# Performance work log

Measured on AMD Instinct MI355X. Metric: run time of the kernel, lower is better.

## Reference

```python
import jax, jax.numpy as jnp
import numpy as np

EPS = 1e-5  # BatchNorm eps (eval mode, running_mean=0, running_var=1)


def conv1x1(x, w):
    # x: [n,c,h,w], w: [o,c]
    return jnp.einsum('nchw,oc->nohw', x, w)


def bn_relu(x, s, b):
    scale = s / jnp.sqrt(1.0 + EPS)
    return jax.nn.relu(x * scale[None, :, None, None] + b[None, :, None, None])


def upsample_bilinear_ac(x, out_h, out_w):
    # nn.Upsample(mode='bilinear', align_corners=True)
    n, c, h, w = x.shape
    ys = jnp.linspace(0.0, h - 1.0, out_h)
    xs = jnp.linspace(0.0, w - 1.0, out_w)
    y0 = jnp.floor(ys).astype(jnp.int32)
    y1 = jnp.minimum(y0 + 1, h - 1)
    x0 = jnp.floor(xs).astype(jnp.int32)
    x1 = jnp.minimum(x0 + 1, w - 1)
    wy = (ys - y0)[None, None, :, None]
    wx = (xs - x0)[None, None, None, :]
    rows = x[:, :, y0, :] * (1.0 - wy) + x[:, :, y1, :] * wy
    return rows[:, :, :, x0] * (1.0 - wx) + rows[:, :, :, x1] * wx


def to_patches(x, ph, pw):
    # [n,c,H,W] -> [n,c,P,L], P = (H//ph)*(W//pw) patches, L = ph*pw pixels
    n, c, H, W = x.shape
    gh, gw = H // ph, W // pw
    return x.reshape(n, c, gh, ph, gw, pw).transpose(0, 1, 2, 4, 3, 5).reshape(n, c, gh * gw, ph * pw)


def from_patches(x, H, W, ph, pw):
    n, c, P, L = x.shape
    gh, gw = H // ph, W // pw
    return x.reshape(n, c, gh, gw, ph, pw).transpose(0, 1, 2, 4, 3, 5).reshape(n, c, H, W)


def patch_attention(q, k, v, ph, pw, H, W):
    qp = to_patches(q, ph, pw)
    kp = to_patches(k, ph, pw)
    vp = to_patches(v, ph, pw)
    # patch-vs-patch similarity, contracted over pixels within a patch
    sim = jax.nn.sigmoid(jnp.einsum('ncpl,ncql->ncpq', qp, kp))
    # sim1 (mean over key patches) + sim2 (mean over query patches), both [n,c,P,1]
    gate = sim.mean(axis=3, keepdims=True) + sim.mean(axis=2)[..., None]
    return from_patches(gate * vp, H, W, ph, pw)


def setup_inputs() -> dict:
    key = jax.random.key(0)
    ks = jax.random.split(key, 20)
    N, Ch, Cl, neck = 8, 256, 512, 64
    H = W = 128
    Hs = Ws = 32
    sc = 0.05
    return {
        'branch0_feats': jax.random.normal(ks[0], (N, Ch, H, W), jnp.float32),
        'other_feats': jax.random.normal(ks[1], (N, Cl, Hs, Ws), jnp.float32),
        'wq1': jax.random.normal(ks[2], (neck, Ch), jnp.float32) * sc,
        'bnq1_s': jax.random.uniform(ks[3], (neck,), jnp.float32, 0.5, 1.5),
        'bnq1_b': jax.random.normal(ks[4], (neck,), jnp.float32) * 0.1,
        'wk1': jax.random.normal(ks[5], (neck, Cl), jnp.float32) * sc,
        'bnk1_s': jax.random.uniform(ks[6], (neck,), jnp.float32, 0.5, 1.5),
        'bnk1_b': jax.random.normal(ks[7], (neck,), jnp.float32) * 0.1,
        'wv1': jax.random.normal(ks[8], (neck, Ch), jnp.float32) * sc,
        'wq2': jax.random.normal(ks[9], (neck, Ch), jnp.float32) * sc,
        'bnq2_s': jax.random.uniform(ks[10], (neck,), jnp.float32, 0.5, 1.5),
        'bnq2_b': jax.random.normal(ks[11], (neck,), jnp.float32) * 0.1,
        'wk2': jax.random.normal(ks[12], (neck, Cl), jnp.float32) * sc,
        'bnk2_s': jax.random.uniform(ks[13], (neck,), jnp.float32, 0.5, 1.5),
        'bnk2_b': jax.random.normal(ks[14], (neck,), jnp.float32) * 0.1,
        'wz': jax.random.normal(ks[15], (Ch, 2 * neck), jnp.float32) * sc,
        'alpha': jax.random.uniform(ks[16], (1,), jnp.float32),
        'gamma': jax.random.uniform(ks[17], (1,), jnp.float32),
    }


def reference(branch0_feats, other_feats, wq1, bnq1_s, bnq1_b, wk1, bnk1_s, bnk1_b, wv1,
              wq2, bnq2_s, bnq2_b, wk2, bnk2_s, bnk2_b, wz, alpha, gamma):
    _, _, H, W = branch0_feats.shape
    _, _, Hs, Ws = other_feats.shape

    value = conv1x1(branch0_feats, wv1)
    query = bn_relu(conv1x1(branch0_feats, wq1), bnq1_s, bnq1_b)
    key = upsample_bilinear_ac(bn_relu(conv1x1(other_feats, wk1), bnk1_s, bnk1_b), H, W)

    half = query.shape[1] // 2
    # scale 1: patches of size (Hs, Ws)
    ctx0 = patch_attention(query[:, :half], key[:, :half], value[:, :half], Hs, Ws, H, W)
    # scale 2: patches of size (Hs//2, Ws//2)
    ctx2 = patch_attention(query[:, half:], key[:, half:], value[:, half:], Hs // 2, Ws // 2, H, W)

    # dense per-pixel sigmoid gating branch
    query2 = bn_relu(conv1x1(branch0_feats, wq2), bnq2_s, bnq2_b)
    key2 = upsample_bilinear_ac(bn_relu(conv1x1(other_feats, wk2), bnk2_s, bnk2_b), H, W)
    ctx3 = value * jax.nn.sigmoid(query2 * key2)

    context = jnp.concatenate([alpha[0] * jnp.concatenate([ctx0, ctx2], axis=1),
                               gamma[0] * ctx3], axis=1)
    return conv1x1(context, wz)
```

## Files before the change

### kernel.cpp

```cpp
#include <hip/hip_runtime.h>
#include <math.h>
#include <stdint.h>

#define N_    8
#define CH    256
#define CL    512
#define NECK  64
#define H_    128
#define W_    128
#define HW    16384
#define HWS   1024
#define EPSB  1e-5f
#define SC31  (31.0f/127.0f)

typedef unsigned short ushort_t;
typedef __attribute__((ext_vector_type(8))) short bf16x8;
typedef __attribute__((ext_vector_type(4))) float f32x4;

union bfpack { ushort_t u[8]; bf16x8 v; };

__device__ __forceinline__ float sigmoidf_(float x){ return 1.0f/(1.0f + __expf(-x)); }

__device__ __forceinline__ ushort_t f2bf(float x){
    union { float f; uint32_t u; } v; v.f = x;
    uint32_t r = (v.u + 0x7FFFu + ((v.u >> 16) & 1u)) >> 16;
    return (ushort_t)r;
}
__device__ __forceinline__ float bf2f(ushort_t b){
    union { uint32_t u; float f; } v; v.u = ((uint32_t)b) << 16;
    return v.f;
}

__device__ __forceinline__ void gload16(const void* g, void* l){
    __builtin_amdgcn_global_load_lds((const __attribute__((address_space(1))) void*)g,
                                     (__attribute__((address_space(3))) void*)l, 16, 0, 0);
}

__global__ __launch_bounds__(256) void k_conv_small_prep(
    const float* __restrict__ x,
    const float* __restrict__ wk1, const float* __restrict__ wk2,
    const float* __restrict__ sk1, const float* __restrict__ bk1,
    const float* __restrict__ sk2, const float* __restrict__ bk2,
    const float* __restrict__ wv1, const float* __restrict__ wq1, const float* __restrict__ wq2,
    const float* __restrict__ wz,
    float* __restrict__ k1small, float* __restrict__ k2small,
    ushort_t* __restrict__ Wbig, ushort_t* __restrict__ Wzb)
{
    __shared__ float xt[64][64];
    __shared__ float wt[64][132];
    if (blockIdx.x >= 128){
        int t = (blockIdx.x - 128)*256 + threadIdx.x;
        if (t < 49152){
            int o = t >> 8, c = t & 255;
            const float* w = (o < 64) ? (wv1 + (size_t)o*CH)
                           : (o < 128) ? (wq1 + (size_t)(o-64)*CH)
                                       : (wq2 + (size_t)(o-128)*CH);
            Wbig[t] = f2bf(w[c]);
        } else {
            int i = t - 49152;
            Wzb[i] = f2bf(wz[i]);
        }
        return;
    }
    int T = blockIdx.x;
    int n = T >> 4;
    int pix0 = (T & 15) * 64;
    int t = threadIdx.x;
    int to = t >> 4;
    int tp = t & 15;
    float acc[8][4];
    #pragma unroll
    for (int i=0;i<8;i++){ acc[i][0]=0.f;acc[i][1]=0.f;acc[i][2]=0.f;acc[i][3]=0.f; }

    const float* xb = x + (size_t)n*CL*HWS + pix0;
    for (int cc=0; cc<8; ++cc){
        #pragma unroll
        for (int i=0;i<16;i++){
            int e = i*256 + t;
            int c = e >> 6, p = e & 63;
            xt[c][p] = xb[(size_t)(cc*64 + c)*HWS + p];
        }
        #pragma unroll
        for (int i=0;i<32;i++){
            int e = i*256 + t;
            int o = e >> 6, c = e & 63;
            const float* wsrc = (o < 64) ? (wk1 + (size_t)o*CL) : (wk2 + (size_t)(o-64)*CL);
            wt[c][o] = wsrc[cc*64 + c];
        }
        __syncthreads();
        #pragma unroll 4
        for (int c=0;c<64;c++){
            float4 xv = *(const float4*)&xt[c][tp*4];
            const float4* wr = (const float4*)&wt[c][to*8];
            float4 wa = wr[0], wb = wr[1];
            float wv[8] = {wa.x,wa.y,wa.z,wa.w, wb.x,wb.y,wb.z,wb.w};
            #pragma unroll
            for (int i=0;i<8;i++){
                acc[i][0] = fmaf(wv[i], xv.x, acc[i][0]);
                acc[i][1] = fmaf(wv[i], xv.y, acc[i][1]);
                acc[i][2] = fmaf(wv[i], xv.z, acc[i][2]);
                acc[i][3] = fmaf(wv[i], xv.w, acc[i][3]);
            }
        }
        __syncthreads();
    }
    float inv = rsqrtf(1.0f + EPSB);
    #pragma unroll
    for (int i=0;i<8;i++){
        int o = to*8 + i;
        int g = o >> 6, oc = o & 63;
        float sc = (g ? sk2[oc] : sk1[oc]) * inv;
        float bb =  g ? bk2[oc] : bk1[oc];
        float4 r;
        r.x = fmaxf(fmaf(acc[i][0],sc,bb), 0.f);
        r.y = fmaxf(fmaf(acc[i][1],sc,bb), 0.f);
        r.z = fmaxf(fmaf(acc[i][2],sc,bb), 0.f);
        r.w = fmaxf(fmaf(acc[i][3],sc,bb), 0.f);
        float* dst = g ? k2small : k1small;
        *(float4*)&dst[(size_t)(n*NECK + oc)*HWS + pix0 + tp*4] = r;
    }
}

__global__ __launch_bounds__(512) void k_gemm_big(
    const float* __restrict__ x,
    const ushort_t* __restrict__ Wb,
    const float* __restrict__ s1, const float* __restrict__ b1,
    const float* __restrict__ s2, const float* __restrict__ b2,
    ushort_t* __restrict__ value, ushort_t* __restrict__ query, ushort_t* __restrict__ query2)
{
    __shared__ ushort_t At[192*64];
    __shared__ ushort_t Bt[128*64];
    int blk = blockIdx.x;
    int n = blk >> 7;
    int pix0 = (blk & 127) << 7;
    int t = threadIdx.x;
    int lane = t & 63;
    int w8 = t >> 6;
    int wm = w8 >> 1, wn = w8 & 1;

    f32x4 acc[3][4];
    #pragma unroll
    for (int m=0;m<3;m++)
        #pragma unroll
        for (int nn=0;nn<4;nn++) acc[m][nn] = (f32x4){0.f,0.f,0.f,0.f};

    const float* xb = x + (size_t)n*CH*HW + pix0;
    float va[8], vb[8];
    {
        const float* xc = xb + (size_t)(8*w8)*HW;
        #pragma unroll
        for (int j=0;j<8;j++){
            va[j] = xc[(size_t)j*HW + lane];
            vb[j] = xc[(size_t)j*HW + 64 + lane];
        }
    }
    for (int kt=0; kt<4; ++kt){
        int c0 = kt*64;
        #pragma unroll
        for (int i=0;i<3;i++){
            int g = i*512 + t;
            int s = g ^ ((g>>3)&7);
            gload16(Wb + (size_t)(s>>3)*CH + c0 + (s&7)*8, (char*)At + g*16);
        }
        uint32_t pa[4], pb[4];
        #pragma unroll
        for (int j=0;j<4;j++){
            pa[j] = (uint32_t)f2bf(va[2*j]) | ((uint32_t)f2bf(va[2*j+1]) << 16);
            pb[j] = (uint32_t)f2bf(vb[2*j]) | ((uint32_t)f2bf(vb[2*j+1]) << 16);
        }
        int c2 = (8*w8)*2;
        int offA = (lane*128 + c2) ^ ((lane&7)<<4);
        int offB = ((lane+64)*128 + c2) ^ ((lane&7)<<4);
        *(uint4*)((char*)Bt + offA) = make_uint4(pa[0],pa[1],pa[2],pa[3]);
        *(uint4*)((char*)Bt + offB) = make_uint4(pb[0],pb[1],pb[2],pb[3]);
        __syncthreads();
        if (kt < 3){
            const float* xc = xb + (size_t)((kt+1)*64 + 8*w8)*HW;
            #pragma unroll
            for (int j=0;j<8;j++){
                va[j] = xc[(size_t)j*HW + lane];
                vb[j] = xc[(size_t)j*HW + 64 + lane];
            }
        }
        #pragma unroll
        for (int ks=0; ks<2; ++ks){
            bf16x8 a[3], b[4];
            #pragma unroll
            for (int m=0;m<3;m++){
                int row = wm*48 + m*16 + (lane&15);
                int off = (row*128 + ks*64 + (lane>>4)*16) ^ ((row&7)<<4);
                a[m] = *(const bf16x8*)((const char*)At + off);
            }
            #pragma unroll
            for (int nn=0;nn<4;nn++){
                int row = wn*64 + nn*16 + (lane&15);
                int off = (row*128 + ks*64 + (lane>>4)*16) ^ ((row&7)<<4);
                b[nn] = *(const bf16x8*)((const char*)Bt + off);
            }
            #pragma unroll
            for (int m=0;m<3;m++)
                #pragma unroll
                for (int nn=0;nn<4;nn++)
                    acc[m][nn] = __builtin_amdgcn_mfma_f32_16x16x32_bf16(a[m], b[nn], acc[m][nn], 0, 0, 0);
        }
        __syncthreads();
    }
    float inv = rsqrtf(1.0f + EPSB);
    #pragma unroll
    for (int m=0;m<3;m++){
        int obase = wm*48 + m*16 + ((lane>>4)<<2);
        #pragma unroll
        for (int r=0;r<4;r++){
            int o = obase + r;
            int grp = o >> 6, oc = o & 63;
            float sc = 1.f, bb = 0.f;
            ushort_t* dst;
            if (grp == 0) dst = value;
            else if (grp == 1){ sc = s1[oc]*inv; bb = b1[oc]; dst = query; }
            else              { sc = s2[oc]*inv; bb = b2[oc]; dst = query2; }
            #pragma unroll
            for (int nn=0;nn<4;nn++){
                int pix = pix0 + wn*64 + nn*16 + (lane&15);
                float v = acc[m][nn][r];
                if (grp) v = fmaxf(fmaf(v, sc, bb), 0.f);
                dst[((size_t)(n*NECK + oc))*HW + pix] = f2bf(v);
            }
        }
    }
}

__global__ __launch_bounds__(256) void k_gates(
    const ushort_t* __restrict__ query, const float* __restrict__ k1small,
    float* __restrict__ gate1, float* __restrict__ gate2)
{
    __shared__ __align__(16) char smem[69632];
    int bid = blockIdx.x;
    int t = threadIdx.x;
    int lane = t & 63, wv = t >> 6;
    int r16 = lane & 15, g = lane >> 4;
    float* ksm = (float*)smem;
    ushort_t* qt = (ushort_t*)(smem + 4096);
    ushort_t* kt = (ushort_t*)(smem + 4096 + 32768);

    if (bid < 256){
        int n = bid >> 5, c = bid & 31;
        const float* ks = k1small + (size_t)(n*NECK + c)*HWS;
        #pragma unroll
        for (int i=0;i<4;i++) ksm[i*256+t] = ks[i*256+t];
        __syncthreads();
        const ushort_t* qb = query + (size_t)(n*NECK + c)*HW;
        #pragma unroll
        for (int i=0;i<8;i++){
            int task = i*256 + t;
            int p = task >> 7, c8 = task & 127;
            int ly = c8 >> 2, lx8 = (c8 & 3)*8;
            int h = (p>>2)*32 + ly, w = (p&3)*32 + lx8;
            bf16x8 qv = *(const bf16x8*)(qb + h*W_ + w);
            int off = (p*2048 + c8*16) ^ ((p&7)<<4);
            *(bf16x8*)((char*)qt + off) = qv;
            float yf = h*SC31; int y0=(int)yf; int y1=min(y0+1,31); float fy=yf-(float)y0;
            bfpack pk;
            #pragma unroll
            for (int j=0;j<8;j++){
                int ww = w + j;
                float xf = ww*SC31; int x0=(int)xf; int x1=min(x0+1,31); float fx=xf-(float)x0;
                float a=ksm[y0*32+x0], b=ksm[y0*32+x1], cc=ksm[y1*32+x0], d=ksm[y1*32+x1];
                float r0=a+(b-a)*fx, r1=cc+(d-cc)*fx;
                pk.u[j] = f2bf(r0 + (r1-r0)*fy);
            }
            *(bf16x8*)((char*)kt + off) = pk.v;
        }
        __syncthreads();
        f32x4 acc = (f32x4){0.f,0.f,0.f,0.f};
        #pragma unroll
        for (int k8=0; k8<8; ++k8){
            int l0 = wv*256 + k8*32 + g*8;
            int off = (r16*2048 + l0*2) ^ ((r16&7)<<4);
            bf16x8 av = *(const bf16x8*)((char*)qt + off);
            bf16x8 bv = *(const bf16x8*)((char*)kt + off);
            acc = __builtin_amdgcn_mfma_f32_16x16x32_bf16(av, bv, acc, 0, 0, 0);
        }
        __syncthreads();
        float* pw = (float*)smem;
        #pragma unroll
        for (int r=0;r<4;r++)
            pw[wv*256 + (g*4+r)*16 + r16] = acc[r];
        __syncthreads();
        float* simM = (float*)(smem + 4096);
        float s = pw[t] + pw[256+t] + pw[512+t] + pw[768+t];
        simM[t] = sigmoidf_(s);
        __syncthreads();
        if (t < 16){
            float rs=0.f, cs=0.f;
            #pragma unroll
            for (int q=0;q<16;q++) rs += simM[t*16+q];
            #pragma unroll
            for (int p=0;p<16;p++) cs += simM[p*16+t];
            gate1[(size_t)(n*32 + c)*16 + t] = (rs + cs) * (1.0f/16.0f);
        }
    } else {
        int b2 = bid - 256;
        int n = b2 >> 5, cl = b2 & 31, c = 32 + cl;
        const float* ks = k1small + (size_t)(n*NECK + c)*HWS;
        #pragma unroll
        for (int i=0;i<4;i++) ksm[i*256+t] = ks[i*256+t];
        __syncthreads();
        const ushort_t* qb = query + (size_t)(n*NECK + c)*HW;
        #pragma unroll
        for (int i=0;i<8;i++){
            int task = i*256 + t;
            int p = task >> 5, c8 = task & 31;
            int ly = c8 >> 1, lx8 = (c8 & 1)*8;
            int h = (p>>3)*16 + ly, w = (p&7)*16 + lx8;
            bf16x8 qv = *(const bf16x8*)(qb + h*W_ + w);
            int off = (p*512 + c8*16) ^ ((p&7)<<4);
            *(bf16x8*)((char*)qt + off) = qv;
            float yf = h*SC31; int y0=(int)yf; int y1=min(y0+1,31); float fy=yf-(float)y0;
            bfpack pk;
            #pragma unroll
            for (int j=0;j<8;j++){
                int ww = w + j;
                float xf = ww*SC31; int x0=(int)xf; int x1=min(x0+1,31); float fx=xf-(float)x0;
                float a=ksm[y0*32+x0], b=ksm[y0*32+x1], cc=ksm[y1*32+x0], d=ksm[y1*32+x1];
                float r0=a+(b-a)*fx, r1=cc+(d-cc)*fx;
                pk.u[j] = f2bf(r0 + (r1-r0)*fy);
            }
            *(bf16x8*)((char*)kt + off) = pk.v;
        }
        __syncthreads();
        f32x4 acc2[4];
        #pragma unroll
        for (int qc=0;qc<4;qc++) acc2[qc] = (f32x4){0.f,0.f,0.f,0.f};
        #pragma unroll
        for (int k8=0; k8<8; ++k8){
            int l0 = k8*32 + g*8;
            int offA = ((wv*16 + r16)*512 + l0*2) ^ ((r16&7)<<4);
            bf16x8 av = *(const bf16x8*)((char*)qt + offA);
            #pragma unroll
            for (int qc=0;qc<4;qc++){
                int offB = ((qc*16 + r16)*512 + l0*2) ^ ((r16&7)<<4);
                bf16x8 bv = *(const bf16x8*)((char*)kt + offB);
                acc2[qc] = __builtin_amdgcn_mfma_f32_16x16x32_bf16(av, bv, acc2[qc], 0, 0, 0);
            }
        }
        __syncthreads();
        float* simM = (float*)smem;
        #pragma unroll
        for (int qc=0;qc<4;qc++)
            #pragma unroll
            for (int r=0;r<4;r++){
                int p = wv*16 + g*4 + r, q = qc*16 + r16;
                simM[p*65 + q] = sigmoidf_(acc2[qc][r]);
            }
        __syncthreads();
        if (t < 64){
            float rs=0.f, cs=0.f;
            for (int q=0;q<64;q++) rs += simM[t*65 + q];
            for (int p=0;p<64;p++) cs += simM[p*65 + t];
            gate2[(size_t)(n*32 + cl)*64 + t] = (rs + cs) * (1.0f/64.0f);
        }
    }
}

__global__ __launch_bounds__(512, 4) void k_final_mfma(
    const ushort_t* __restrict__ value, const ushort_t* __restrict__ query2,
    const float* __restrict__ k2small,
    const float* __restrict__ gate1, const float* __restrict__ gate2,
    const ushort_t* __restrict__ Wzb,
    const float* __restrict__ alpha_p, const float* __restrict__ gamma_p,
    float* __restrict__ out)
{
    __shared__ __align__(16) char smem[59392];
    ushort_t* Ct = (ushort_t*)smem;
    float* g1s = (float*)(smem + 32768);
    float* g2s = (float*)(smem + 34816);
    float* k2r = (float*)(smem + 43008);
    int blk = blockIdx.x;
    int n = blk >> 7, h = blk & 127;
    int pix0 = h << 7;
    int t = threadIdx.x;
    int lane = t & 63;
    int wid = t >> 6;
    int wm = wid >> 1, wn = wid & 1;

    int px = t & 127, qd = t >> 7;
    const size_t vbase = (size_t)n*NECK*HW + pix0 + px;
    ushort_t vreg[16], qreg[16];
    #pragma unroll
    for (int i=0;i<16;i++){
        int c = qd*16 + i;
        vreg[i] = value [vbase + (size_t)c*HW];
        qreg[i] = query2[vbase + (size_t)c*HW];
    }

    float alpha = alpha_p[0], gamma = gamma_p[0];
    g1s[t & 511] = gate1[(size_t)n*512 + (t & 511)];
    #pragma unroll
    for (int i=0;i<4;i++) g2s[i*512 + t] = gate2[(size_t)n*2048 + i*512 + t];

    float yf = h * SC31;
    int y0 = (int)yf, y1 = min(y0+1, 31);
    float fy = yf - (float)y0;
    #pragma unroll
    for (int i=0;i<8;i++){
        int e = i*512 + t;
        int buf = e >> 11, c = (e >> 5) & 63, xx = e & 31;
        k2r[buf*2048 + c*32 + xx] = k2small[((size_t)n*NECK + c)*HWS + (buf ? y1 : y0)*32 + xx];
    }
    __syncthreads();

    float xf = px * SC31;
    int x0 = (int)xf, x1 = min(x0+1, 31);
    float fx = xf - (float)x0;
    int patch1 = (h>>5)*4 + (px>>5);
    int patch2 = (h>>4)*8 + (px>>4);
    #pragma unroll
    for (int j=0;j<2;j++){
        bfpack pk;
        #pragma unroll
        for (int i=0;i<8;i++){
            int ch = qd*16 + j*8 + i;
            float g = (ch < 32) ? g1s[ch*16 + patch1] : g2s[(ch-32)*64 + patch2];
            pk.u[i] = f2bf(alpha * g * bf2f(vreg[j*8+i]));
        }
        int off = (px*256 + qd*32 + j*16) ^ ((px&7)<<4);
        *(bf16x8*)((char*)Ct + off) = pk.v;
    }
    #pragma unroll
    for (int j=0;j<2;j++){
        bfpack pk;
        #pragma unroll
        for (int i=0;i<8;i++){
            int c = qd*16 + j*8 + i;
            float vv = bf2f(vreg[j*8+i]);
            float q2 = bf2f(qreg[j*8+i]);
            float r0 = k2r[c*32+x0];      r0 += (k2r[c*32+x1] - r0)*fx;
            float r1 = k2r[2048+c*32+x0]; r1 += (k2r[2048+c*32+x1] - r1)*fx;
            float kv = r0 + (r1 - r0)*fy;
            pk.u[i] = f2bf(gamma * vv * sigmoidf_(q2*kv));
        }
        int off = (px*256 + 128 + qd*32 + j*16) ^ ((px&7)<<4);
        *(bf16x8*)((char*)Ct + off) = pk.v;
    }
    __syncthreads();

    f32x4 acc[4][4];
    #pragma unroll
    for (int m=0;m<4;m++)
        #pragma unroll
        for (int nn=0;nn<4;nn++) acc[m][nn] = (f32x4){0.f,0.f,0.f,0.f};
    #pragma unroll
    for (int ks=0; ks<4; ++ks){
        bf16x8 a[4], b[4];
        #pragma unroll
        for (int m=0;m<4;m++){
            int row = wm*64 + m*16 + (lane&15);
            a[m] = *(const bf16x8*)(Wzb + row*128 + ks*32 + (lane>>4)*8);
        }
        #pragma unroll
        for (int nn=0;nn<4;nn++){
            int row = wn*64 + nn*16 + (lane&15);
            int off = (row*256 + ks*64 + (lane>>4)*16) ^ ((row&7)<<4);
            b[nn] = *(const bf16x8*)((const char*)Ct + off);
        }
        #pragma unroll
        for (int m=0;m<4;m++)
            #pragma unroll
            for (int nn=0;nn<4;nn++)
                acc[m][nn] = __builtin_amdgcn_mfma_f32_16x16x32_bf16(a[m], b[nn], acc[m][nn], 0, 0, 0);
    }

    #pragma unroll
    for (int m=0;m<4;m++){
        int obase = wm*64 + m*16 + ((lane>>4)<<2);
        #pragma unroll
        for (int r=0;r<4;r++){
            int o = obase + r;
            float* dst = out + ((size_t)(n*CH + o))*HW + pix0 + wn*64 + (lane&15);
            #pragma unroll
            for (int nn=0;nn<4;nn++)
                dst[nn*16] = acc[m][nn][r];
        }
    }
}

extern "C" void kernel_launch(void* const* d_in, const int* in_sizes, int n_in,
                              void* d_out, int out_size, void* d_ws, size_t ws_size,
                              hipStream_t stream) {
    const float* x0  = (const float*)d_in[0];
    const float* xo  = (const float*)d_in[1];
    const float* wq1 = (const float*)d_in[2];
    const float* s1  = (const float*)d_in[3];
    const float* b1  = (const float*)d_in[4];
    const float* wk1 = (const float*)d_in[5];
    const float* sk1 = (const float*)d_in[6];
    const float* bk1 = (const float*)d_in[7];
    const float* wv1 = (const float*)d_in[8];
    const float* wq2 = (const float*)d_in[9];
    const float* s2  = (const float*)d_in[10];
    const float* b2  = (const float*)d_in[11];
    const float* wk2 = (const float*)d_in[12];
    const float* sk2 = (const float*)d_in[13];
    const float* bk2 = (const float*)d_in[14];
    const float* wz  = (const float*)d_in[15];
    const float* alp = (const float*)d_in[16];
    const float* gam = (const float*)d_in[17];

    ushort_t* value  = (ushort_t*)d_ws;
    ushort_t* query  = value  + 8388608;
    ushort_t* query2 = query  + 8388608;
    float*    k1s    = (float*)(query2 + 8388608);
    float*    k2s    = k1s + 524288;
    float*    g1     = k2s + 524288;
    float*    g2     = g1 + 4096;
    ushort_t* Wbig   = (ushort_t*)(g2 + 16384);
    ushort_t* Wzb    = Wbig + 49152;

    k_conv_small_prep<<<dim3(448), dim3(256), 0, stream>>>(
        xo, wk1, wk2, sk1, bk1, sk2, bk2, wv1, wq1, wq2, wz, k1s, k2s, Wbig, Wzb);
    k_gemm_big<<<dim3(1024), dim3(512), 0, stream>>>(
        x0, Wbig, s1, b1, s2, b2, value, query, query2);
    k_gates<<<dim3(512), dim3(256), 0, stream>>>(query, k1s, g1, g2);
    k_final_mfma<<<dim3(1024), dim3(512), 0, stream>>>(value, query2, k2s, g1, g2, Wzb,
                                                       alp, gam, (float*)d_out);
}
```

Measured before the change: 153.3 us.

## Merge small conv, big GEMM and weight prep into one phase-1 kernel

Fuses the small key convolutions, the weight bf16 conversion and the large value/query GEMM into a single launch, using block-index ranges to pick the role. The big GEMM now loads fp32 weights directly and converts them in registers instead of reading a prebuilt bf16 weight buffer, which removes the dependency on a prep kernel. The small key convolution moves from fp32 FMA to bf16 MFMA. This saves one launch and a serial dependency, and costs redundant weight conversion in every block plus reduced precision for the key path.

```diff
diff --git a/kernel.cpp b/kernel.cpp
--- a/kernel.cpp
+++ b/kernel.cpp
@@ -1,4 +1,5 @@
 #include <hip/hip_runtime.h>
+#include <hip/hip_bf16.h>
 #include <math.h>
 #include <stdint.h>
 
@@ -22,121 +23,149 @@
 __device__ __forceinline__ float sigmoidf_(float x){ return 1.0f/(1.0f + __expf(-x)); }
 
 __device__ __forceinline__ ushort_t f2bf(float x){
-    union { float f; uint32_t u; } v; v.f = x;
-    uint32_t r = (v.u + 0x7FFFu + ((v.u >> 16) & 1u)) >> 16;
-    return (ushort_t)r;
+    union { __hip_bfloat16 h; ushort_t u; } cv;
+    cv.h = __float2bfloat16(x);
+    return cv.u;
+}
+__device__ __forceinline__ uint32_t pack2(float lo, float hi){
+    return (uint32_t)f2bf(lo) | ((uint32_t)f2bf(hi) << 16);
 }
 __device__ __forceinline__ float bf2f(ushort_t b){
     union { uint32_t u; float f; } v; v.u = ((uint32_t)b) << 16;
     return v.f;
 }
 
-__device__ __forceinline__ void gload16(const void* g, void* l){
-    __builtin_amdgcn_global_load_lds((const __attribute__((address_space(1))) void*)g,
-                                     (__attribute__((address_space(3))) void*)l, 16, 0, 0);
-}
-
-__global__ __launch_bounds__(256) void k_conv_small_prep(
+__global__ __launch_bounds__(512) void k_phase1(
     const float* __restrict__ x,
+    const float* __restrict__ xo,
+    const float* __restrict__ wv1, const float* __restrict__ wq1, const float* __restrict__ wq2,
     const float* __restrict__ wk1, const float* __restrict__ wk2,
+    const float* __restrict__ s1, const float* __restrict__ b1,
+    const float* __restrict__ s2, const float* __restrict__ b2,
     const float* __restrict__ sk1, const float* __restrict__ bk1,
     const float* __restrict__ sk2, const float* __restrict__ bk2,
-    const float* __restrict__ wv1, const float* __restrict__ wq1, const float* __restrict__ wq2,
     const float* __restrict__ wz,
-    float* __restrict__ k1small, float* __restrict__ k2small,
-    ushort_t* __restrict__ Wbig, ushort_t* __restrict__ Wzb)
+    ushort_t* __restrict__ value, ushort_t* __restrict__ query, ushort_t* __restrict__ query2,
+    float* __restrict__ k1s, float* __restrict__ k2s, ushort_t* __restrict__ Wzb)
 {
-    __shared__ float xt[64][64];
-    __shared__ float wt[64][132];
-    if (blockIdx.x >= 128){
-        int t = (blockIdx.x - 128)*256 + threadIdx.x;
-        if (t < 49152){
-            int o = t >> 8, c = t & 255;
-            const float* w = (o < 64) ? (wv1 + (size_t)o*CH)
-                           : (o < 128) ? (wq1 + (size_t)(o-64)*CH)
-                                       : (wq2 + (size_t)(o-128)*CH);
-            Wbig[t] = f2bf(w[c]);
-        } else {
-            int i = t - 49152;
-            Wzb[i] = f2bf(wz[i]);
-        }
+    __shared__ __align__(16) char smem[40960];
+    int blk = blockIdx.x;
+    int t = threadIdx.x;
+
+    if (blk >= 1088){
+        int i = (blk - 1088)*2048 + t*4;
+        float4 f = *(const float4*)(wz + i);
+        *(uint2*)(Wzb + i) = make_uint2(pack2(f.x,f.y), pack2(f.z,f.w));
         return;
     }
-    int T = blockIdx.x;
-    int n = T >> 4;
-    int pix0 = (T & 15) * 64;
-    int t = threadIdx.x;
-    int to = t >> 4;
-    int tp = t & 15;
-    float acc[8][4];
-    #pragma unroll
-    for (int i=0;i<8;i++){ acc[i][0]=0.f;acc[i][1]=0.f;acc[i][2]=0.f;acc[i][3]=0.f; }
-
-    const float* xb = x + (size_t)n*CL*HWS + pix0;
-    for (int cc=0; cc<8; ++cc){
-        #pragma unroll
-        for (int i=0;i<16;i++){
-            int e = i*256 + t;
-            int c = e >> 6, p = e & 63;
-            xt[c][p] = xb[(size_t)(cc*64 + c)*HWS + p];
-        }
-        #pragma unroll
-        for (int i=0;i<32;i++){
-            int e = i*256 + t;
-            int o = e >> 6, c = e & 63;
-            const float* wsrc = (o < 64) ? (wk1 + (size_t)o*CL) : (wk2 + (size_t)(o-64)*CL);
-            wt[c][o] = wsrc[cc*64 + c];
-        }
-        __syncthreads();
-        #pragma unroll 4
-        for (int c=0;c<64;c++){
-            float4 xv = *(const float4*)&xt[c][tp*4];
-            const float4* wr = (const float4*)&wt[c][to*8];
-            float4 wa = wr[0], wb = wr[1];
-            float wv[8] = {wa.x,wa.y,wa.z,wa.w, wb.x,wb.y,wb.z,wb.w};
-            #pragma unroll
-            for (int i=0;i<8;i++){
-                acc[i][0] = fmaf(wv[i], xv.x, acc[i][0]);
-                acc[i][1] = fmaf(wv[i], xv.y, acc[i][1]);
-                acc[i][2] = fmaf(wv[i], xv.z, acc[i][2]);
-                acc[i][3] = fmaf(wv[i], xv.w, acc[i][3]);
-            }
-        }
-        __syncthreads();
-    }
+
+    int lane = t & 63, w8 = t >> 6;
+    int wm = w8 >> 1, wn = w8 & 1;
+    int r16 = lane & 15;
     float inv = rsqrtf(1.0f + EPSB);
-    #pragma unroll
-    for (int i=0;i<8;i++){
-        int o = to*8 + i;
-        int g = o >> 6, oc = o & 63;
-        float sc = (g ? sk2[oc] : sk1[oc]) * inv;
-        float bb =  g ? bk2[oc] : bk1[oc];
-        float4 r;
-        r.x = fmaxf(fmaf(acc[i][0],sc,bb), 0.f);
-        r.y = fmaxf(fmaf(acc[i][1],sc,bb), 0.f);
-        r.z = fmaxf(fmaf(acc[i][2],sc,bb), 0.f);
-        r.w = fmaxf(fmaf(acc[i][3],sc,bb), 0.f);
-        float* dst = g ? k2small : k1small;
-        *(float4*)&dst[(size_t)(n*NECK + oc)*HWS + pix0 + tp*4] = r;
-    }
-}
-
-__global__ __launch_bounds__(512) void k_gemm_big(
-    const float* __restrict__ x,
-    const ushort_t* __restrict__ Wb,
-    const float* __restrict__ s1, const float* __restrict__ b1,
-    const float* __restrict__ s2, const float* __restrict__ b2,
-    ushort_t* __restrict__ value, ushort_t* __restrict__ query, ushort_t* __restrict__ query2)
-{
-    __shared__ ushort_t At[192*64];
-    __shared__ ushort_t Bt[128*64];
-    int blk = blockIdx.x;
+
+    if (blk >= 1024){
+        ushort_t* At = (ushort_t*)smem;
+        ushort_t* Bt = (ushort_t*)(smem + 16384);
+        int b = blk - 1024;
+        int n = b >> 3, pix0 = (b & 7) << 7;
+        f32x4 acc[2][4];
+        #pragma unroll
+        for (int m=0;m<2;m++)
+            #pragma unroll
+            for (int nn=0;nn<4;nn++) acc[m][nn] = (f32x4){0.f,0.f,0.f,0.f};
+
+        const float* xb = xo + (size_t)n*CL*HWS + pix0;
+        float va[8], vb[8];
+        {
+            const float* xc = xb + (size_t)(8*w8)*HWS;
+            #pragma unroll
+            for (int j=0;j<8;j++){
+                va[j] = xc[(size_t)j*HWS + lane];
+                vb[j] = xc[(size_t)j*HWS + 64 + lane];
+            }
+        }
+        int oo = t >> 3, c8 = t & 7;
+        for (int kt=0; kt<8; ++kt){
+            int c0 = kt*64;
+            const float* ws0 = wk1 + (size_t)oo*CL + c0 + c8*8;
+            const float* ws1 = wk2 + (size_t)oo*CL + c0 + c8*8;
+            float4 a00 = *(const float4*)ws0, a01 = *(const float4*)(ws0+4);
+            float4 a10 = *(const float4*)ws1, a11 = *(const float4*)(ws1+4);
+            uint32_t pa[4], pb[4];
+            #pragma unroll
+            for (int j=0;j<4;j++){
+                pa[j] = pack2(va[2*j], va[2*j+1]);
+                pb[j] = pack2(vb[2*j], vb[2*j+1]);
+            }
+            int offA = (lane*128 + w8*16) ^ ((lane&7)<<4);
+            int offB = ((lane+64)*128 + w8*16) ^ ((lane&7)<<4);
+            *(uint4*)((char*)Bt + offA) = make_uint4(pa[0],pa[1],pa[2],pa[3]);
+            *(uint4*)((char*)Bt + offB) = make_uint4(pb[0],pb[1],pb[2],pb[3]);
+            {
+                int off0 = (oo*128 + c8*16) ^ ((oo&7)<<4);
+                int off1 = ((64+oo)*128 + c8*16) ^ ((oo&7)<<4);
+                *(uint4*)((char*)At + off0) = make_uint4(pack2(a00.x,a00.y),pack2(a00.z,a00.w),
+                                                         pack2(a01.x,a01.y),pack2(a01.z,a01.w));
+                *(uint4*)((char*)At + off1) = make_uint4(pack2(a10.x,a10.y),pack2(a10.z,a10.w),
+                                                         pack2(a11.x,a11.y),pack2(a11.z,a11.w));
+            }
+            __syncthreads();
+            if (kt < 7){
+                const float* xc = xb + (size_t)((kt+1)*64 + 8*w8)*HWS;
+                #pragma unroll
+                for (int j=0;j<8;j++){
+                    va[j] = xc[(size_t)j*HWS + lane];
+                    vb[j] = xc[(size_t)j*HWS + 64 + lane];
+                }
+            }
+            #pragma unroll
+            for (int ks=0; ks<2; ++ks){
+                bf16x8 a[2], bfr[4];
+                #pragma unroll
+                for (int m=0;m<2;m++){
+                    int row = wm*32 + m*16 + r16;
+                    int off = (row*128 + ks*64 + (lane>>4)*16) ^ ((row&7)<<4);
+                    a[m] = *(const bf16x8*)((const char*)At + off);
+                }
+                #pragma unroll
+                for (int nn=0;nn<4;nn++){
+                    int row = wn*64 + nn*16 + r16;
+                    int off = (row*128 + ks*64 + (lane>>4)*16) ^ ((row&7)<<4);
+                    bfr[nn] = *(const bf16x8*)((const char*)Bt + off);
+                }
+                #pragma unroll
+                for (int m=0;m<2;m++)
+                    #pragma unroll
+                    for (int nn=0;nn<4;nn++)
+                        acc[m][nn] = __builtin_amdgcn_mfma_f32_16x16x32_bf16(a[m], bfr[nn], acc[m][nn], 0, 0, 0);
+            }
+            __syncthreads();
+        }
+        #pragma unroll
+        for (int m=0;m<2;m++){
+            int obase = wm*32 + m*16 + ((lane>>4)<<2);
+            #pragma unroll
+            for (int r=0;r<4;r++){
+                int o = obase + r;
+                int oc = o & 63;
+                float sc = ((o<64) ? sk1[oc] : sk2[oc]) * inv;
+                float bb =  (o<64) ? bk1[oc] : bk2[oc];
+                float* dst = ((o<64) ? k1s : k2s) + ((size_t)n*NECK + oc)*HWS + pix0;
+                #pragma unroll
+                for (int nn=0;nn<4;nn++){
+                    int px = wn*64 + nn*16 + r16;
+                    dst[px] = fmaxf(fmaf(acc[m][nn][r], sc, bb), 0.f);
+                }
+            }
+        }
+        return;
+    }
+
+    ushort_t* At = (ushort_t*)smem;
+    ushort_t* Bt = (ushort_t*)(smem + 24576);
     int n = blk >> 7;
     int pix0 = (blk & 127) << 7;
-    int t = threadIdx.x;
-    int lane = t & 63;
-    int w8 = t >> 6;
-    int wm = w8 >> 1, wn = w8 & 1;
 
     f32x4 acc[3][4];
     #pragma unroll
@@ -154,25 +183,38 @@
             vb[j] = xc[(size_t)j*HW + 64 + lane];
         }
     }
+    int oo = t >> 3, c8 = t & 7;
     for (int kt=0; kt<4; ++kt){
         int c0 = kt*64;
-        #pragma unroll
-        for (int i=0;i<3;i++){
-            int g = i*512 + t;
-            int s = g ^ ((g>>3)&7);
-            gload16(Wb + (size_t)(s>>3)*CH + c0 + (s&7)*8, (char*)At + g*16);
-        }
+        const float* ws0 = wv1 + (size_t)oo*CH + c0 + c8*8;
+        const float* ws1 = wq1 + (size_t)oo*CH + c0 + c8*8;
+        const float* ws2 = wq2 + (size_t)oo*CH + c0 + c8*8;
+        float4 a00 = *(const float4*)ws0, a01 = *(const float4*)(ws0+4);
+        float4 a10 = *(const float4*)ws1, a11 = *(const float4*)(ws1+4);
+        float4 a20 = *(const float4*)ws2, a21 = *(const float4*)(ws2+4);
         uint32_t pa[4], pb[4];
         #pragma unroll
         for (int j=0;j<4;j++){
-            pa[j] = (uint32_t)f2bf(va[2*j]) | ((uint32_t)f2bf(va[2*j+1]) << 16);
-            pb[j] = (uint32_t)f2bf(vb[2*j]) | ((uint32_t)f2bf(vb[2*j+1]) << 16);
-        }
-        int c2 = (8*w8)*2;
+            pa[j] = pack2(va[2*j], va[2*j+1]);
+            pb[j] = pack2(vb[2*j], vb[2*j+1]);
+        }
+        int c2 = w8*16;
         int offA = (lane*128 + c2) ^ ((lane&7)<<4);
         int offB = ((lane+64)*128 + c2) ^ ((lane&7)<<4);
         *(uint4*)((char*)Bt + offA) = make_uint4(pa[0],pa[1],pa[2],pa[3]);
         *(uint4*)((char*)Bt + offB) = make_uint4(pb[0],pb[1],pb[2],pb[3]);
+        {
+            int swz = (oo&7)<<4;
+            int off0 = ((oo     )*128 + c8*16) ^ swz;
+            int off1 = ((oo + 64)*128 + c8*16) ^ swz;
+            int off2 = ((oo +128)*128 + c8*16) ^ swz;
+            *(uint4*)((char*)At + off0) = make_uint4(pack2(a00.x,a00.y),pack2(a00.z,a00.w),
+                                                     pack2(a01.x,a01.y),pack2(a01.z,a01.w));
+            *(uint4*)((char*)At + off1) = make_uint4(pack2(a10.x,a10.y),pack2(a10.z,a10.w),
+                                                     pack2(a11.x,a11.y),pack2(a11.z,a11.w));
+            *(uint4*)((char*)At + off2) = make_uint4(pack2(a20.x,a20.y),pack2(a20.z,a20.w),
+                                                     pack2(a21.x,a21.y),pack2(a21.z,a21.w));
+        }
         __syncthreads();
         if (kt < 3){
             const float* xc = xb + (size_t)((kt+1)*64 + 8*w8)*HW;
@@ -184,28 +226,27 @@
         }
         #pragma unroll
         for (int ks=0; ks<2; ++ks){
-            bf16x8 a[3], b[4];
+            bf16x8 a[3], bfr[4];
             #pragma unroll
             for (int m=0;m<3;m++){
-                int row = wm*48 + m*16 + (lane&15);
+                int row = wm*48 + m*16 + r16;
                 int off = (row*128 + ks*64 + (lane>>4)*16) ^ ((row&7)<<4);
                 a[m] = *(const bf16x8*)((const char*)At + off);
             }
             #pragma unroll
             for (int nn=0;nn<4;nn++){
-                int row = wn*64 + nn*16 + (lane&15);
+                int row = wn*64 + nn*16 + r16;
                 int off = (row*128 + ks*64 + (lane>>4)*16) ^ ((row&7)<<4);
-                b[nn] = *(const bf16x8*)((const char*)Bt + off);
+                bfr[nn] = *(const bf16x8*)((const char*)Bt + off);
             }
             #pragma unroll
             for (int m=0;m<3;m++)
                 #pragma unroll
                 for (int nn=0;nn<4;nn++)
-                    acc[m][nn] = __builtin_amdgcn_mfma_f32_16x16x32_bf16(a[m], b[nn], acc[m][nn], 0, 0, 0);
-        }
-        __syncthreads();
-    }
-    float inv = rsqrtf(1.0f + EPSB);
+                    acc[m][nn] = __builtin_amdgcn_mfma_f32_16x16x32_bf16(a[m], bfr[nn], acc[m][nn], 0, 0, 0);
+        }
+        __syncthreads();
+    }
     #pragma unroll
     for (int m=0;m<3;m++){
         int obase = wm*48 + m*16 + ((lane>>4)<<2);
@@ -220,7 +261,7 @@
             else              { sc = s2[oc]*inv; bb = b2[oc]; dst = query2; }
             #pragma unroll
             for (int nn=0;nn<4;nn++){
-                int pix = pix0 + wn*64 + nn*16 + (lane&15);
+                int pix = pix0 + wn*64 + nn*16 + r16;
                 float v = acc[m][nn][r];
                 if (grp) v = fmaxf(fmaf(v, sc, bb), 0.f);
                 dst[((size_t)(n*NECK + oc))*HW + pix] = f2bf(v);
@@ -513,13 +554,11 @@
     float*    k2s    = k1s + 524288;
     float*    g1     = k2s + 524288;
     float*    g2     = g1 + 4096;
-    ushort_t* Wbig   = (ushort_t*)(g2 + 16384);
-    ushort_t* Wzb    = Wbig + 49152;
-
-    k_conv_small_prep<<<dim3(448), dim3(256), 0, stream>>>(
-        xo, wk1, wk2, sk1, bk1, sk2, bk2, wv1, wq1, wq2, wz, k1s, k2s, Wbig, Wzb);
-    k_gemm_big<<<dim3(1024), dim3(512), 0, stream>>>(
-        x0, Wbig, s1, b1, s2, b2, value, query, query2);
+    ushort_t* Wzb    = (ushort_t*)(g2 + 16384);
+
+    k_phase1<<<dim3(1104), dim3(512), 0, stream>>>(
+        x0, xo, wv1, wq1, wq2, wk1, wk2, s1, b1, s2, b2, sk1, bk1, sk2, bk2, wz,
+        value, query, query2, k1s, k2s, Wzb);
     k_gates<<<dim3(512), dim3(256), 0, stream>>>(query, k1s, g1, g2);
     k_final_mfma<<<dim3(1024), dim3(512), 0, stream>>>(value, query2, k2s, g1, g2, Wzb,
                                                        alp, gam, (float*)d_out);
```

Measured after the change: 127.8 us. 16.6% less time.
